# Optimization experiments

Hardware: AMD Instinct MI355X
Metric: run time of the kernel (lower is better)

Reference implementation:

```python
import jax, jax.numpy as jnp
import numpy as np

B, N, D, NFP, L = 4096, 64, 128, 2048, 3  # graphs, nodes/graph, emb_dim, vocab, layers


def setup_inputs() -> dict:
    key = jax.random.key(0)
    k0, k1, k2, k3, k4 = jax.random.split(key, 5)
    fps = jax.random.randint(k0, (B * N,), 0, NFP)            # node fingerprint ids, all graphs concatenated
    adj = jax.random.uniform(k1, (B, N, N), dtype=jnp.float32)  # per-graph adjacency blocks
    emb = jax.random.normal(k2, (NFP, D), dtype=jnp.float32) * 0.02
    W = jax.random.normal(k3, (L, D, D), dtype=jnp.float32) / np.sqrt(D).astype(np.float32)
    b = jax.random.normal(k4, (L, D), dtype=jnp.float32) * 0.01
    return {"fps": fps, "adj": adj, "emb": emb, "W": W, "b": b}


def reference(fps, adj, emb, W, b):
    # h = self.emb(fps): gather, then view as [B, N, D] so the block-diagonal
    # adjs.mm becomes an exact batched matmul over the true graph blocks.
    h = emb[fps].reshape(B, N, D)
    for l in range(L):
        # z = relu(W_l h + b_l); torch Linear is x @ W^T + b
        z = jax.nn.relu(jnp.einsum('bnd,kd->bnk', h, W[l]) + b[l])
        # h = z + adjs.mm(z), restricted to the diagonal blocks (same math)
        h = z + jnp.einsum('bmn,bnd->bmd', adj, z)
    # split by sz_list and sum each chunk -> per-graph sum pooling
    return h.sum(axis=1)  # [B, D]
```

## Files before the change

kernel.cpp:

```cpp
#include <hip/hip_runtime.h>

#define NGRAPH 4096
#define NNODE  64
#define NDIM   128
#define NLAYER 3
#define PH 136
#define PZ 72

typedef __attribute__((ext_vector_type(8))) short short8;
typedef __attribute__((ext_vector_type(4))) float f32x4;
typedef __bf16 bf16x2 __attribute__((ext_vector_type(2)));

__device__ __align__(16) ushort g_wbf[NLAYER * NDIM * NDIM];

static __device__ inline ushort f2bf(float f) {
  unsigned u = __float_as_uint(f);
  u += 0x7FFF + ((u >> 16) & 1);
  return (ushort)(u >> 16);
}

static __device__ inline unsigned pkbf(float x, float y) {
#if __has_builtin(__builtin_amdgcn_cvt_pk_bf16_f32)
  bf16x2 v = __builtin_amdgcn_cvt_pk_bf16_f32(x, y);
  return __builtin_bit_cast(unsigned, v);
#else
  return (unsigned)f2bf(x) | ((unsigned)f2bf(y) << 16);
#endif
}

__global__ __launch_bounds__(256) void convert_w(const float* __restrict__ W) {
  int i = blockIdx.x * 256 + threadIdx.x;
  g_wbf[i] = f2bf(W[i]);
}

__global__ __launch_bounds__(256, 4) void mpnn_mfma(
    const int* __restrict__ fps, const float* __restrict__ adj,
    const float* __restrict__ emb, const float* __restrict__ bias,
    float* __restrict__ out) {
  __shared__ __align__(16) ushort sh[NNODE * PH];
  __shared__ __align__(16) ushort szT[NDIM * PZ];

  const int g    = blockIdx.x;
  const int t    = threadIdx.x;
  const int w    = t >> 6;
  const int lane = t & 63;
  const int r    = lane & 15;
  const int q    = lane >> 4;
  const int n0   = w << 5;

  const int* fg = fps + g * NNODE;
#pragma unroll
  for (int it = 0; it < 8; ++it) {
    int idx = it * 256 + t;
    int n = idx >> 5;
    int c = (idx & 31) << 2;
    float4 v = *(const float4*)(emb + fg[n] * NDIM + c);
    uint2 u = {pkbf(v.x, v.y), pkbf(v.z, v.w)};
    *(uint2*)(sh + n * PH + c) = u;
  }

  const float* adjg = adj + (size_t)g * NNODE * NNODE;
  short8 fadj[4][2];
  union S8 { short8 s8; unsigned d[4]; };
#pragma unroll
  for (int nt = 0; nt < 4; ++nt) {
    int row = nt * 16 + r;
    const float* rp = adjg + row * NNODE;
#pragma unroll
    for (int kh = 0; kh < 2; ++kh) {
      int cb = kh * 32 + 8 * q;
      float4 v0 = *(const float4*)(rp + cb);
      float4 v1 = *(const float4*)(rp + cb + 4);
      float vv[8] = {v0.x, v0.y, v0.z, v0.w, v1.x, v1.y, v1.z, v1.w};
      if ((nt >> 1) == kh) {
#pragma unroll
        for (int j = 0; j < 8; ++j)
          if (row == cb + j) vv[j] += 1.0f;
      }
      S8 hi;
#pragma unroll
      for (int jp = 0; jp < 4; ++jp) hi.d[jp] = pkbf(vv[2 * jp], vv[2 * jp + 1]);
      fadj[nt][kh] = hi.s8;
    }
  }
  __syncthreads();

  for (int l = 0; l < NLAYER; ++l) {
    const ushort* Wl = g_wbf + l * NDIM * NDIM;
    const float*  bl = bias + l * NDIM;

    f32x4 acc[4][2];
#pragma unroll
    for (int nt = 0; nt < 2; ++nt) {
      float bv = bl[n0 + nt * 16 + r];
#pragma unroll
      for (int mt = 0; mt < 4; ++mt) acc[mt][nt] = (f32x4){bv, bv, bv, bv};
    }
#pragma unroll
    for (int k0 = 0; k0 < NDIM; k0 += 32) {
      short8 bw0 = *(const short8*)(Wl + (n0 + r) * NDIM + k0 + 8 * q);
      short8 bw1 = *(const short8*)(Wl + (n0 + 16 + r) * NDIM + k0 + 8 * q);
#pragma unroll
      for (int mt = 0; mt < 4; ++mt) {
        short8 ah = *(const short8*)(sh + (mt * 16 + r) * PH + k0 + 8 * q);
        acc[mt][0] = __builtin_amdgcn_mfma_f32_16x16x32_bf16(ah, bw0, acc[mt][0], 0, 0, 0);
        acc[mt][1] = __builtin_amdgcn_mfma_f32_16x16x32_bf16(ah, bw1, acc[mt][1], 0, 0, 0);
      }
    }
#pragma unroll
    for (int mt = 0; mt < 4; ++mt)
#pragma unroll
      for (int nt = 0; nt < 2; ++nt) {
        f32x4 a = acc[mt][nt];
        uint2 u = {pkbf(fmaxf(a[0], 0.f), fmaxf(a[1], 0.f)),
                   pkbf(fmaxf(a[2], 0.f), fmaxf(a[3], 0.f))};
        *(uint2*)(szT + (n0 + nt * 16 + r) * PZ + mt * 16 + 4 * q) = u;
      }

    f32x4 acc2[2][4];
#pragma unroll
    for (int mt = 0; mt < 2; ++mt)
#pragma unroll
      for (int nt = 0; nt < 4; ++nt) acc2[mt][nt] = (f32x4){0.f, 0.f, 0.f, 0.f};
#pragma unroll
    for (int kh = 0; kh < 2; ++kh) {
#pragma unroll
      for (int mt = 0; mt < 2; ++mt) {
        short8 az = *(const short8*)(szT + (n0 + mt * 16 + r) * PZ + kh * 32 + 8 * q);
#pragma unroll
        for (int nt = 0; nt < 4; ++nt)
          acc2[mt][nt] = __builtin_amdgcn_mfma_f32_16x16x32_bf16(az, fadj[nt][kh], acc2[mt][nt], 0, 0, 0);
      }
    }

    if (l < NLAYER - 1) {
      __syncthreads();
#pragma unroll
      for (int mt = 0; mt < 2; ++mt)
#pragma unroll
        for (int nt = 0; nt < 4; ++nt) {
          f32x4 a = acc2[mt][nt];
          uint2 u = {pkbf(a[0], a[1]), pkbf(a[2], a[3])};
          *(uint2*)(sh + (nt * 16 + r) * PH + n0 + mt * 16 + 4 * q) = u;
        }
      __syncthreads();
    } else {
#pragma unroll
      for (int mt = 0; mt < 2; ++mt) {
        f32x4 s;
#pragma unroll
        for (int i = 0; i < 4; ++i)
          s[i] = acc2[mt][0][i] + acc2[mt][1][i] + acc2[mt][2][i] + acc2[mt][3][i];
#pragma unroll
        for (int m = 1; m <= 8; m <<= 1) {
          s[0] += __shfl_xor(s[0], m);
          s[1] += __shfl_xor(s[1], m);
          s[2] += __shfl_xor(s[2], m);
          s[3] += __shfl_xor(s[3], m);
        }
        if (r == 0) {
          float4 o = {s[0], s[1], s[2], s[3]};
          *(float4*)(out + (size_t)g * NDIM + n0 + mt * 16 + 4 * q) = o;
        }
      }
    }
  }
}

extern "C" void kernel_launch(void* const* d_in, const int* in_sizes, int n_in,
                              void* d_out, int out_size, void* d_ws, size_t ws_size,
                              hipStream_t stream) {
  const int*   fps  = (const int*)d_in[0];
  const float* adj  = (const float*)d_in[1];
  const float* emb  = (const float*)d_in[2];
  const float* W    = (const float*)d_in[3];
  const float* bias = (const float*)d_in[4];
  float* out = (float*)d_out;

  hipLaunchKernelGGL(convert_w, dim3(192), dim3(256), 0, stream, W);
  hipLaunchKernelGGL(mpnn_mfma, dim3(NGRAPH), dim3(256), 0, stream,
                     fps, adj, emb, bias, out);
}
```

Baseline: 176.8 us.

## Pass relu output via lane permutes and double-buffer node features in LDS

The relu(Wh+b) tile no longer goes through a transposed shared-memory buffer. Each wave keeps it in registers and rebuilds the MFMA A-operand layout with ds_bpermute lane shuffles. Node features now ping-pong between two LDS buffers, which removes one of the two block barriers per layer, and all bias values are loaded once before the layer loop. The cost is more permute instructions, with bpermute still using the LDS crossbar, plus extra registers for the packed z values and biases.

```diff
diff --git a/kernel.cpp b/kernel.cpp
--- a/kernel.cpp
+++ b/kernel.cpp
@@ -5,13 +5,12 @@
 #define NDIM   128
 #define NLAYER 3
 #define PH 136
-#define PZ 72
 
 typedef __attribute__((ext_vector_type(8))) short short8;
 typedef __attribute__((ext_vector_type(4))) float f32x4;
 typedef __bf16 bf16x2 __attribute__((ext_vector_type(2)));
 
-__device__ __align__(16) ushort g_wbf[NLAYER * NDIM * NDIM];
+union S8 { short8 s8; unsigned d[4]; };
 
 static __device__ inline ushort f2bf(float f) {
   unsigned u = __float_as_uint(f);
@@ -28,6 +27,8 @@
 #endif
 }
 
+__device__ __align__(16) ushort g_wbf[NLAYER * NDIM * NDIM];
+
 __global__ __launch_bounds__(256) void convert_w(const float* __restrict__ W) {
   int i = blockIdx.x * 256 + threadIdx.x;
   g_wbf[i] = f2bf(W[i]);
@@ -37,8 +38,8 @@
     const int* __restrict__ fps, const float* __restrict__ adj,
     const float* __restrict__ emb, const float* __restrict__ bias,
     float* __restrict__ out) {
-  __shared__ __align__(16) ushort sh[NNODE * PH];
-  __shared__ __align__(16) ushort szT[NDIM * PZ];
+  __shared__ __align__(16) ushort sh0[NNODE * PH];
+  __shared__ __align__(16) ushort sh1[NNODE * PH];
 
   const int g    = blockIdx.x;
   const int t    = threadIdx.x;
@@ -48,6 +49,10 @@
   const int q    = lane >> 4;
   const int n0   = w << 5;
 
+  const int addr0 = (r + 32 * (q & 1)) << 2;
+  const int addr1 = addr0 + 64;
+  const bool hiQ  = (q >= 2);
+
   const int* fg = fps + g * NNODE;
 #pragma unroll
   for (int it = 0; it < 8; ++it) {
@@ -56,12 +61,11 @@
     int c = (idx & 31) << 2;
     float4 v = *(const float4*)(emb + fg[n] * NDIM + c);
     uint2 u = {pkbf(v.x, v.y), pkbf(v.z, v.w)};
-    *(uint2*)(sh + n * PH + c) = u;
+    *(uint2*)(sh0 + n * PH + c) = u;
   }
 
   const float* adjg = adj + (size_t)g * NNODE * NNODE;
   short8 fadj[4][2];
-  union S8 { short8 s8; unsigned d[4]; };
 #pragma unroll
   for (int nt = 0; nt < 4; ++nt) {
     int row = nt * 16 + r;
@@ -83,18 +87,27 @@
       fadj[nt][kh] = hi.s8;
     }
   }
+
+  float bv[NLAYER][2];
+#pragma unroll
+  for (int l = 0; l < NLAYER; ++l)
+#pragma unroll
+    for (int nt = 0; nt < 2; ++nt) bv[l][nt] = bias[l * NDIM + n0 + nt * 16 + r];
+
   __syncthreads();
 
+#pragma unroll 1
   for (int l = 0; l < NLAYER; ++l) {
-    const ushort* Wl = g_wbf + l * NDIM * NDIM;
-    const float*  bl = bias + l * NDIM;
+    const ushort* shr = (l & 1) ? sh1 : sh0;
+    ushort*       shw = (l & 1) ? sh0 : sh1;
+    const ushort* Wl  = g_wbf + l * NDIM * NDIM;
 
     f32x4 acc[4][2];
 #pragma unroll
     for (int nt = 0; nt < 2; ++nt) {
-      float bv = bl[n0 + nt * 16 + r];
-#pragma unroll
-      for (int mt = 0; mt < 4; ++mt) acc[mt][nt] = (f32x4){bv, bv, bv, bv};
+      float b = bv[l][nt];
+#pragma unroll
+      for (int mt = 0; mt < 4; ++mt) acc[mt][nt] = (f32x4){b, b, b, b};
     }
 #pragma unroll
     for (int k0 = 0; k0 < NDIM; k0 += 32) {
@@ -102,19 +115,19 @@
       short8 bw1 = *(const short8*)(Wl + (n0 + 16 + r) * NDIM + k0 + 8 * q);
 #pragma unroll
       for (int mt = 0; mt < 4; ++mt) {
-        short8 ah = *(const short8*)(sh + (mt * 16 + r) * PH + k0 + 8 * q);
+        short8 ah = *(const short8*)(shr + (mt * 16 + r) * PH + k0 + 8 * q);
         acc[mt][0] = __builtin_amdgcn_mfma_f32_16x16x32_bf16(ah, bw0, acc[mt][0], 0, 0, 0);
         acc[mt][1] = __builtin_amdgcn_mfma_f32_16x16x32_bf16(ah, bw1, acc[mt][1], 0, 0, 0);
       }
     }
+    unsigned zc[4][2][2];
 #pragma unroll
     for (int mt = 0; mt < 4; ++mt)
 #pragma unroll
       for (int nt = 0; nt < 2; ++nt) {
         f32x4 a = acc[mt][nt];
-        uint2 u = {pkbf(fmaxf(a[0], 0.f), fmaxf(a[1], 0.f)),
-                   pkbf(fmaxf(a[2], 0.f), fmaxf(a[3], 0.f))};
-        *(uint2*)(szT + (n0 + nt * 16 + r) * PZ + mt * 16 + 4 * q) = u;
+        zc[mt][nt][0] = pkbf(fmaxf(a[0], 0.f), fmaxf(a[1], 0.f));
+        zc[mt][nt][1] = pkbf(fmaxf(a[2], 0.f), fmaxf(a[3], 0.f));
       }
 
     f32x4 acc2[2][4];
@@ -125,32 +138,40 @@
 #pragma unroll
     for (int kh = 0; kh < 2; ++kh) {
 #pragma unroll
-      for (int mt = 0; mt < 2; ++mt) {
-        short8 az = *(const short8*)(szT + (n0 + mt * 16 + r) * PZ + kh * 32 + 8 * q);
+      for (int mt2 = 0; mt2 < 2; ++mt2) {
+        S8 az;
+#pragma unroll
+        for (int p = 0; p < 4; ++p) {
+          int comp = p & 1;
+          int lo = __builtin_amdgcn_ds_bpermute((p < 2) ? addr0 : addr1,
+                                                (int)zc[2 * kh][mt2][comp]);
+          int hi = __builtin_amdgcn_ds_bpermute((p < 2) ? addr0 : addr1,
+                                                (int)zc[2 * kh + 1][mt2][comp]);
+          az.d[p] = (unsigned)(hiQ ? hi : lo);
+        }
 #pragma unroll
         for (int nt = 0; nt < 4; ++nt)
-          acc2[mt][nt] = __builtin_amdgcn_mfma_f32_16x16x32_bf16(az, fadj[nt][kh], acc2[mt][nt], 0, 0, 0);
+          acc2[mt2][nt] = __builtin_amdgcn_mfma_f32_16x16x32_bf16(az.s8, fadj[nt][kh], acc2[mt2][nt], 0, 0, 0);
       }
     }
 
     if (l < NLAYER - 1) {
-      __syncthreads();
-#pragma unroll
-      for (int mt = 0; mt < 2; ++mt)
+#pragma unroll
+      for (int mt2 = 0; mt2 < 2; ++mt2)
 #pragma unroll
         for (int nt = 0; nt < 4; ++nt) {
-          f32x4 a = acc2[mt][nt];
+          f32x4 a = acc2[mt2][nt];
           uint2 u = {pkbf(a[0], a[1]), pkbf(a[2], a[3])};
-          *(uint2*)(sh + (nt * 16 + r) * PH + n0 + mt * 16 + 4 * q) = u;
+          *(uint2*)(shw + (nt * 16 + r) * PH + n0 + mt2 * 16 + 4 * q) = u;
         }
       __syncthreads();
     } else {
 #pragma unroll
-      for (int mt = 0; mt < 2; ++mt) {
+      for (int mt2 = 0; mt2 < 2; ++mt2) {
         f32x4 s;
 #pragma unroll
         for (int i = 0; i < 4; ++i)
-          s[i] = acc2[mt][0][i] + acc2[mt][1][i] + acc2[mt][2][i] + acc2[mt][3][i];
+          s[i] = acc2[mt2][0][i] + acc2[mt2][1][i] + acc2[mt2][2][i] + acc2[mt2][3][i];
 #pragma unroll
         for (int m = 1; m <= 8; m <<= 1) {
           s[0] += __shfl_xor(s[0], m);
@@ -160,7 +181,7 @@
         }
         if (r == 0) {
           float4 o = {s[0], s[1], s[2], s[3]};
-          *(float4*)(out + (size_t)g * NDIM + n0 + mt * 16 + 4 * q) = o;
+          *(float4*)(out + (size_t)g * NDIM + n0 + mt2 * 16 + 4 * q) = o;
         }
       }
     }
```

Result: no change. 175.0 us (-1.0%).
